# Performance work log

Hardware: AMD Instinct MI355X
Metric: run time of the kernel (lower is better)

The kernel has to match this reference:

```python
import jax, jax.numpy as jnp
import numpy as np

D_MODEL = 1024
N_HEADS = 16
D_HEAD = D_MODEL // N_HEADS
WINDOW = 128
D_FF = 3 * D_MODEL
EPS = 1e-5


def _layer_norm(x, g, b):
    mu = jnp.mean(x, axis=-1, keepdims=True)
    var = jnp.var(x, axis=-1, keepdims=True)
    return (x - mu) * jax.lax.rsqrt(var + EPS) * g + b


def setup_inputs() -> dict:
    key = jax.random.key(0)
    ks = jax.random.split(key, 10)
    B, S = 2, 2048
    sd = 0.02
    return {
        "x": jax.random.normal(ks[0], (B, S, D_MODEL), dtype=jnp.float32),
        "w_qkv": jax.random.normal(ks[1], (D_MODEL, 3 * D_MODEL), dtype=jnp.float32) * sd,
        "b_qkv": jnp.zeros((3 * D_MODEL,), jnp.float32),
        "w_out": jax.random.normal(ks[2], (D_MODEL, D_MODEL), dtype=jnp.float32) * sd,
        "b_out": jnp.zeros((D_MODEL,), jnp.float32),
        "w_ff1": jax.random.normal(ks[3], (D_MODEL, D_FF), dtype=jnp.float32) * sd,
        "b_ff1": jnp.zeros((D_FF,), jnp.float32),
        "w_ff2": jax.random.normal(ks[4], (D_FF, D_MODEL), dtype=jnp.float32) * sd,
        "b_ff2": jnp.zeros((D_MODEL,), jnp.float32),
        "ln1_g": jnp.ones((D_MODEL,), jnp.float32),
        "ln1_b": jnp.zeros((D_MODEL,), jnp.float32),
        "ln2_g": jnp.ones((D_MODEL,), jnp.float32),
        "ln2_b": jnp.zeros((D_MODEL,), jnp.float32),
    }


def reference(x, w_qkv, b_qkv, w_out, b_out, w_ff1, b_ff1, w_ff2, b_ff2,
              ln1_g, ln1_b, ln2_g, ln2_b):
    B, S, D = x.shape
    h = _layer_norm(x, ln1_g, ln1_b)
    qkv = (h @ w_qkv + b_qkv).reshape(B, S, 3, N_HEADS, D_HEAD)
    q, k, v = (jnp.moveaxis(qkv[:, :, i], 1, 2) for i in range(3))  # (B,H,S,dh)
    scores = jnp.einsum('bhqd,bhkd->bhqk', q, k) / jnp.sqrt(jnp.float32(D_HEAD))
    i = jnp.arange(S)[:, None]
    j = jnp.arange(S)[None, :]
    allowed = (j <= i) & (j > i - WINDOW)  # causal sliding window band
    scores = jnp.where(allowed, scores, -jnp.inf)
    attn = jax.nn.softmax(scores, axis=-1)
    ctx = jnp.einsum('bhqk,bhkd->bqhd', attn, v).reshape(B, S, D)
    x = x + (ctx @ w_out + b_out)
    h2 = _layer_norm(x, ln2_g, ln2_b)
    ff = jax.nn.gelu(h2 @ w_ff1 + b_ff1, approximate=False) @ w_ff2 + b_ff2
    return x + ff
```

## Files before the change

### kernel.cpp

```cpp
#include <hip/hip_runtime.h>

#define D_MODEL 1024
#define SEQ 2048
#define BATCH 2
#define NH 16
#define DH 64
#define WIN 128
#define DFF 3072

typedef __bf16 bf16x8 __attribute__((ext_vector_type(8)));
typedef float f32x4 __attribute__((ext_vector_type(4)));
typedef unsigned short u16;
typedef unsigned int u32;

__device__ __forceinline__ float b2f(u16 u) {
    unsigned int x = ((unsigned int)u) << 16;
    return __uint_as_float(x);
}
__device__ __forceinline__ u16 f2b(float f) {
    unsigned int x = __float_as_uint(f);
    x += 0x7fffu + ((x >> 16) & 1u);
    return (u16)(x >> 16);
}
__device__ __forceinline__ u32 pk2(float a, float b) {
    return (u32)f2b(a) | ((u32)f2b(b) << 16);
}

__global__ __launch_bounds__(256) void transpose_cvt_k(
        const float* __restrict__ in, u16* __restrict__ out, int R, int C) {
    __shared__ u16 tile[32][33];
    int tx = threadIdx.x & 31;
    int ty = threadIdx.x >> 5;
    int r0 = blockIdx.y * 32, c0 = blockIdx.x * 32;
#pragma unroll
    for (int i = 0; i < 4; ++i)
        tile[ty + i * 8][tx] = f2b(in[(size_t)(r0 + ty + i * 8) * C + c0 + tx]);
    __syncthreads();
#pragma unroll
    for (int i = 0; i < 4; ++i)
        out[(size_t)(c0 + ty + i * 8) * R + r0 + tx] = tile[tx][ty + i * 8];
}

__global__ __launch_bounds__(256) void ln_k(
        const float* __restrict__ x, const float* __restrict__ g,
        const float* __restrict__ bta, u16* __restrict__ out) {
    int row = blockIdx.x;
    const float* xr = x + (size_t)row * D_MODEL;
    float v[4];
    float sum = 0.f, sq = 0.f;
#pragma unroll
    for (int i = 0; i < 4; ++i) {
        v[i] = xr[threadIdx.x + i * 256];
        sum += v[i];
        sq += v[i] * v[i];
    }
#pragma unroll
    for (int off = 32; off > 0; off >>= 1) {
        sum += __shfl_xor(sum, off, 64);
        sq  += __shfl_xor(sq, off, 64);
    }
    __shared__ float s1[4], s2[4];
    int w = threadIdx.x >> 6;
    if ((threadIdx.x & 63) == 0) { s1[w] = sum; s2[w] = sq; }
    __syncthreads();
    sum = s1[0] + s1[1] + s1[2] + s1[3];
    sq  = s2[0] + s2[1] + s2[2] + s2[3];
    float mu = sum * (1.f / D_MODEL);
    float var = sq * (1.f / D_MODEL) - mu * mu;
    float rstd = rsqrtf(var + 1e-5f);
    u16* outr = out + (size_t)row * D_MODEL;
#pragma unroll
    for (int i = 0; i < 4; ++i) {
        int c = threadIdx.x + i * 256;
        outr[c] = f2b((v[i] - mu) * rstd * g[c] + bta[c]);
    }
}

template <int GELU, int RESID, int OUTF32, int VSPLIT>
__global__ __launch_bounds__(256) void gemm_k(
        const u16* __restrict__ A, const u16* __restrict__ Bt,
        const float* __restrict__ bias, const float* __restrict__ resid,
        void* __restrict__ Cv, u16* __restrict__ vt,
        int M, int N, int K, int ldc) {
    __shared__ u16 As[128 * 64];
    __shared__ u16 Bs[128 * 64];
    int tid = threadIdx.x;
    int w = tid >> 6, lane = tid & 63;
    int qd = lane >> 4, l15 = lane & 15;

    int lin = blockIdx.x;
    int xcd = lin & 7, idx = lin >> 3;
    int m0 = (xcd * 4 + (idx & 3)) * 128;
    int n0 = (idx >> 2) * 128;

    const u16* gsrc[8];
    u16* ldst[8];
#pragma unroll
    for (int i = 0; i < 8; ++i) {
        int c = w * 8 + i;
        int cb = c & 15;
        int row = cb * 8 + (lane >> 3);
        int cg = (lane & 7) ^ (row & 7);
        gsrc[i] = (c < 16 ? A + (size_t)(m0 + row) * K
                          : Bt + (size_t)(n0 + row) * K) + cg * 8;
        ldst[i] = (c < 16 ? As : Bs) + cb * 512;
    }

    int wm = w & 1, wn = w >> 1;
    f32x4 acc[4][4];
#pragma unroll
    for (int mt = 0; mt < 4; ++mt)
#pragma unroll
        for (int nt = 0; nt < 4; ++nt)
            acc[mt][nt] = (f32x4){0.f, 0.f, 0.f, 0.f};

    int aoff[4][2], boff[4][2];
#pragma unroll
    for (int t = 0; t < 4; ++t) {
        int ar = wm * 64 + t * 16 + l15;
        int br = wn * 64 + t * 16 + l15;
#pragma unroll
        for (int h = 0; h < 2; ++h) {
            aoff[t][h] = ar * 64 + (((h * 4 + qd) ^ (ar & 7)) * 8);
            boff[t][h] = br * 64 + (((h * 4 + qd) ^ (br & 7)) * 8);
        }
    }

    for (int k0 = 0; k0 < K; k0 += 64) {
        __syncthreads();
#pragma unroll
        for (int i = 0; i < 8; ++i)
            __builtin_amdgcn_global_load_lds(
                (__attribute__((address_space(1))) void*)(gsrc[i] + k0),
                (__attribute__((address_space(3))) void*)(ldst[i]), 16, 0, 0);
        __syncthreads();
        bf16x8 av[4][2], bv[4][2];
#pragma unroll
        for (int t = 0; t < 4; ++t)
#pragma unroll
            for (int h = 0; h < 2; ++h) {
                av[t][h] = *(const bf16x8*)&As[aoff[t][h]];
                bv[t][h] = *(const bf16x8*)&Bs[boff[t][h]];
            }
#pragma unroll
        for (int mt = 0; mt < 4; ++mt)
#pragma unroll
            for (int nt = 0; nt < 4; ++nt) {
                acc[mt][nt] = __builtin_amdgcn_mfma_f32_16x16x32_bf16(
                    av[mt][0], bv[nt][0], acc[mt][nt], 0, 0, 0);
                acc[mt][nt] = __builtin_amdgcn_mfma_f32_16x16x32_bf16(
                    av[mt][1], bv[nt][1], acc[mt][nt], 0, 0, 0);
            }
    }

#pragma unroll
    for (int mt = 0; mt < 4; ++mt) {
        int row0 = m0 + wm * 64 + mt * 16 + qd * 4;
#pragma unroll
        for (int nt = 0; nt < 4; ++nt) {
            int col = n0 + wn * 64 + nt * 16 + l15;
            float v[4];
#pragma unroll
            for (int reg = 0; reg < 4; ++reg) {
                v[reg] = acc[mt][nt][reg] + bias[col];
                if (GELU) v[reg] = 0.5f * v[reg] * (1.f + erff(v[reg] * 0.70710678118654752f));
                if (RESID) v[reg] += resid[(size_t)(row0 + reg) * ldc + col];
            }
            if (VSPLIT && col >= 2 * D_MODEL) {
                int d = col - 2 * D_MODEL;
                int bh = (row0 >> 11) * NH + (d >> 6);
                ushort4 pkv = {f2b(v[0]), f2b(v[1]), f2b(v[2]), f2b(v[3])};
                *(ushort4*)&vt[((size_t)(bh * DH + (d & 63))) * SEQ + (row0 & (SEQ - 1))] = pkv;
            } else {
#pragma unroll
                for (int reg = 0; reg < 4; ++reg) {
                    if (OUTF32) ((float*)Cv)[(size_t)(row0 + reg) * ldc + col] = v[reg];
                    else        ((u16*)Cv)[(size_t)(row0 + reg) * ldc + col] = f2b(v[reg]);
                }
            }
        }
    }
}

__global__ __launch_bounds__(256) void attn_k(
        const u16* __restrict__ qk, const u16* __restrict__ vt,
        u16* __restrict__ ctx) {
    int lane = threadIdx.x & 63, l15 = lane & 15, quad = lane >> 4;
    int t = blockIdx.x * 4 + (threadIdx.x >> 6);
    int qt = t & (SEQ / 16 - 1);
    int h  = (t >> 7) & (NH - 1);
    int b  = t >> 11;
    int q0 = qt * 16;
    int bh = b * NH + h;

    const u16* qrow = qk + (size_t)(b * SEQ + q0 + l15) * (2 * D_MODEL) + h * DH + quad * 8;
    bf16x8 qf0 = *(const bf16x8*)(qrow);
    bf16x8 qf1 = *(const bf16x8*)(qrow + 32);
    const u16* kbase = qk + (size_t)(b * SEQ) * (2 * D_MODEL) + D_MODEL + h * DH + quad * 8;
    const u16* vbase = vt + (size_t)(bh * DH) * SEQ;

    f32x4 o[4] = {{0.f, 0.f, 0.f, 0.f}, {0.f, 0.f, 0.f, 0.f},
                  {0.f, 0.f, 0.f, 0.f}, {0.f, 0.f, 0.f, 0.f}};
    float m = -1e30f, l = 0.f;
    int q = q0 + l15;
    int cs = q0 - (WIN - 1);
    cs = cs < 0 ? 0 : (cs & ~31);

    for (int c = cs; c <= q0 + 15; c += 32) {
        const u16* k0p = kbase + (size_t)(c + l15) * (2 * D_MODEL);
        const u16* k1p = k0p + (size_t)16 * (2 * D_MODEL);
        bf16x8 ka0 = *(const bf16x8*)(k0p);
        bf16x8 ka1 = *(const bf16x8*)(k0p + 32);
        bf16x8 kb0 = *(const bf16x8*)(k1p);
        bf16x8 kb1 = *(const bf16x8*)(k1p + 32);
        f32x4 s0 = {0.f, 0.f, 0.f, 0.f}, s1 = {0.f, 0.f, 0.f, 0.f};
        s0 = __builtin_amdgcn_mfma_f32_16x16x32_bf16(ka0, qf0, s0, 0, 0, 0);
        s0 = __builtin_amdgcn_mfma_f32_16x16x32_bf16(ka1, qf1, s0, 0, 0, 0);
        s1 = __builtin_amdgcn_mfma_f32_16x16x32_bf16(kb0, qf0, s1, 0, 0, 0);
        s1 = __builtin_amdgcn_mfma_f32_16x16x32_bf16(kb1, qf1, s1, 0, 0, 0);

        float p0[4], p1[4];
        float cm = -1e30f;
#pragma unroll
        for (int reg = 0; reg < 4; ++reg) {
            int k0i = c + quad * 4 + reg;
            p0[reg] = ((unsigned)(q - k0i) < WIN) ? s0[reg] * 0.125f : -1e30f;
            p1[reg] = ((unsigned)(q - k0i - 16) < WIN) ? s1[reg] * 0.125f : -1e30f;
            cm = fmaxf(cm, fmaxf(p0[reg], p1[reg]));
        }
        cm = fmaxf(cm, __shfl_xor(cm, 16, 64));
        cm = fmaxf(cm, __shfl_xor(cm, 32, 64));
        float mn = fmaxf(m, cm);
        float alpha = __expf(m - mn);
        m = mn;
        float ls = 0.f;
#pragma unroll
        for (int reg = 0; reg < 4; ++reg) {
            p0[reg] = __expf(p0[reg] - mn);
            p1[reg] = __expf(p1[reg] - mn);
            ls += p0[reg] + p1[reg];
        }
        ls += __shfl_xor(ls, 16, 64);
        ls += __shfl_xor(ls, 32, 64);
        l = l * alpha + ls;
#pragma unroll
        for (int mt = 0; mt < 4; ++mt) o[mt] *= alpha;

        u32 z0 = pk2(p0[0], p0[1]), z1 = pk2(p0[2], p0[3]);
        u32 w0 = pk2(p1[0], p1[1]), w1 = pk2(p1[2], p1[3]);
        int slo = ((quad & 1) * 2) * 16 + l15;
        int shi = slo + 16;
        u32 zl0 = (u32)__shfl((int)z0, slo, 64), zl1 = (u32)__shfl((int)z1, slo, 64);
        u32 zh0 = (u32)__shfl((int)z0, shi, 64), zh1 = (u32)__shfl((int)z1, shi, 64);
        u32 wl0 = (u32)__shfl((int)w0, slo, 64), wl1 = (u32)__shfl((int)w1, slo, 64);
        u32 wh0 = (u32)__shfl((int)w0, shi, 64), wh1 = (u32)__shfl((int)w1, shi, 64);
        alignas(16) u32 pr[4];
        pr[0] = quad < 2 ? zl0 : wl0;
        pr[1] = quad < 2 ? zl1 : wl1;
        pr[2] = quad < 2 ? zh0 : wh0;
        pr[3] = quad < 2 ? zh1 : wh1;
        bf16x8 pf = *(const bf16x8*)pr;

#pragma unroll
        for (int mt = 0; mt < 4; ++mt) {
            bf16x8 vf = *(const bf16x8*)(vbase + (size_t)(mt * 16 + l15) * SEQ + c + quad * 8);
            o[mt] = __builtin_amdgcn_mfma_f32_16x16x32_bf16(vf, pf, o[mt], 0, 0, 0);
        }
    }

    float rdiv = 1.f / l;
    u16* crow = ctx + (size_t)(b * SEQ + q0 + l15) * D_MODEL + h * DH;
#pragma unroll
    for (int mt = 0; mt < 4; ++mt) {
        ushort4 pkv = {f2b(o[mt][0] * rdiv), f2b(o[mt][1] * rdiv),
                       f2b(o[mt][2] * rdiv), f2b(o[mt][3] * rdiv)};
        *(ushort4*)(crow + mt * 16 + quad * 4) = pkv;
    }
}

extern "C" void kernel_launch(void* const* d_in, const int* in_sizes, int n_in,
                              void* d_out, int out_size, void* d_ws, size_t ws_size,
                              hipStream_t stream) {
    (void)in_sizes; (void)n_in; (void)out_size; (void)ws_size;
    const float* x     = (const float*)d_in[0];
    const float* w_qkv = (const float*)d_in[1];
    const float* b_qkv = (const float*)d_in[2];
    const float* w_out = (const float*)d_in[3];
    const float* b_out = (const float*)d_in[4];
    const float* w_ff1 = (const float*)d_in[5];
    const float* b_ff1 = (const float*)d_in[6];
    const float* w_ff2 = (const float*)d_in[7];
    const float* b_ff2 = (const float*)d_in[8];
    const float* ln1g  = (const float*)d_in[9];
    const float* ln1b  = (const float*)d_in[10];
    const float* ln2g  = (const float*)d_in[11];
    const float* ln2b  = (const float*)d_in[12];
    float* out = (float*)d_out;

    const int M = BATCH * SEQ;
    char* base = (char*)d_ws;
    u16*   hbf   = (u16*)(base);
    u16*   qkbuf = (u16*)(base + (8ll  << 20));
    u16*   ctxbf = (u16*)(base + (24ll << 20));
    u16*   vtbuf = (u16*)(base + (32ll << 20));
    u16*   ffbf  = (u16*)(base + (8ll  << 20));
    float* x2    = (float*)(base + (40ll << 20));
    u16*   wqkvT = (u16*)(base + (56ll << 20));
    u16*   woutT = (u16*)(base + (62ll << 20));
    u16*   wff1T = (u16*)(base + (64ll << 20));
    u16*   wff2T = (u16*)(base + (70ll << 20));

    transpose_cvt_k<<<dim3(3 * D_MODEL / 32, D_MODEL / 32), 256, 0, stream>>>(w_qkv, wqkvT, D_MODEL, 3 * D_MODEL);
    transpose_cvt_k<<<dim3(D_MODEL / 32, D_MODEL / 32), 256, 0, stream>>>(w_out, woutT, D_MODEL, D_MODEL);
    transpose_cvt_k<<<dim3(DFF / 32, D_MODEL / 32), 256, 0, stream>>>(w_ff1, wff1T, D_MODEL, DFF);
    transpose_cvt_k<<<dim3(D_MODEL / 32, DFF / 32), 256, 0, stream>>>(w_ff2, wff2T, DFF, D_MODEL);

    ln_k<<<M, 256, 0, stream>>>(x, ln1g, ln1b, hbf);
    gemm_k<0, 0, 0, 1><<<dim3((3 * D_MODEL / 128) * 32), 256, 0, stream>>>(
        hbf, wqkvT, b_qkv, nullptr, qkbuf, vtbuf, M, 3 * D_MODEL, D_MODEL, 2 * D_MODEL);
    attn_k<<<dim3(BATCH * NH * (SEQ / 16) / 4), 256, 0, stream>>>(qkbuf, vtbuf, ctxbf);
    gemm_k<0, 1, 1, 0><<<dim3((D_MODEL / 128) * 32), 256, 0, stream>>>(
        ctxbf, woutT, b_out, x, x2, nullptr, M, D_MODEL, D_MODEL, D_MODEL);
    ln_k<<<M, 256, 0, stream>>>(x2, ln2g, ln2b, hbf);
    gemm_k<1, 0, 0, 0><<<dim3((DFF / 128) * 32), 256, 0, stream>>>(
        hbf, wff1T, b_ff1, nullptr, ffbf, nullptr, M, DFF, D_MODEL, DFF);
    gemm_k<0, 1, 1, 0><<<dim3((D_MODEL / 128) * 32), 256, 0, stream>>>(
        ffbf, wff2T, b_ff2, x2, out, nullptr, M, D_MODEL, DFF, D_MODEL);
}
```

Measured before the change: 314.9 us.

## Pipeline GEMM global-to-LDS loads with a 4-stage K=32 ring buffer

The GEMM main loop now keeps a four-slot LDS ring of 32-wide K slices and prefetches three steps ahead using direct global-to-LDS loads. Partial vmcnt waits and a single barrier per step replace the previous load-then-sync pattern. This is meant to hide global memory latency behind MFMA work. In exchange, each step does half the MFMA work per barrier, and the LDS footprint doubles to 64KB, which may lower occupancy.

```diff
diff --git a/kernel.cpp b/kernel.cpp
--- a/kernel.cpp
+++ b/kernel.cpp
@@ -25,6 +25,10 @@
 __device__ __forceinline__ u32 pk2(float a, float b) {
     return (u32)f2b(a) | ((u32)f2b(b) << 16);
 }
+
+#define WAIT_VMCNT0() __builtin_amdgcn_s_waitcnt(0x0F70)
+#define WAIT_VMCNT4() __builtin_amdgcn_s_waitcnt(0x0F74)
+#define WAIT_VMCNT8() __builtin_amdgcn_s_waitcnt(0x0F78)
 
 __global__ __launch_bounds__(256) void transpose_cvt_k(
         const float* __restrict__ in, u16* __restrict__ out, int R, int C) {
@@ -82,8 +86,8 @@
         const float* __restrict__ bias, const float* __restrict__ resid,
         void* __restrict__ Cv, u16* __restrict__ vt,
         int M, int N, int K, int ldc) {
-    __shared__ u16 As[128 * 64];
-    __shared__ u16 Bs[128 * 64];
+    __shared__ u16 As[4 * 4096];
+    __shared__ u16 Bs[4 * 4096];
     int tid = threadIdx.x;
     int w = tid >> 6, lane = tid & 63;
     int qd = lane >> 4, l15 = lane & 15;
@@ -93,17 +97,17 @@
     int m0 = (xcd * 4 + (idx & 3)) * 128;
     int n0 = (idx >> 2) * 128;
 
-    const u16* gsrc[8];
-    u16* ldst[8];
-#pragma unroll
-    for (int i = 0; i < 8; ++i) {
-        int c = w * 8 + i;
-        int cb = c & 15;
-        int row = cb * 8 + (lane >> 3);
-        int cg = (lane & 7) ^ (row & 7);
-        gsrc[i] = (c < 16 ? A + (size_t)(m0 + row) * K
-                          : Bt + (size_t)(n0 + row) * K) + cg * 8;
-        ldst[i] = (c < 16 ? As : Bs) + cb * 512;
+    const u16* gsrc[4];
+    u16* ldst[4];
+#pragma unroll
+    for (int i = 0; i < 4; ++i) {
+        int c = w * 4 + i;
+        int cb = c & 7;
+        int row = cb * 16 + (lane >> 2);
+        int cg = (lane & 3) ^ ((row >> 1) & 3);
+        gsrc[i] = (c < 8 ? A + (size_t)(m0 + row) * K
+                         : Bt + (size_t)(n0 + row) * K) + cg * 8;
+        ldst[i] = (c < 8 ? As : Bs) + cb * 512;
     }
 
     int wm = w & 1, wn = w >> 1;
@@ -114,43 +118,54 @@
         for (int nt = 0; nt < 4; ++nt)
             acc[mt][nt] = (f32x4){0.f, 0.f, 0.f, 0.f};
 
-    int aoff[4][2], boff[4][2];
+    int aoff[4], boff[4];
 #pragma unroll
     for (int t = 0; t < 4; ++t) {
         int ar = wm * 64 + t * 16 + l15;
         int br = wn * 64 + t * 16 + l15;
-#pragma unroll
-        for (int h = 0; h < 2; ++h) {
-            aoff[t][h] = ar * 64 + (((h * 4 + qd) ^ (ar & 7)) * 8);
-            boff[t][h] = br * 64 + (((h * 4 + qd) ^ (br & 7)) * 8);
-        }
-    }
-
-    for (int k0 = 0; k0 < K; k0 += 64) {
-        __syncthreads();
-#pragma unroll
-        for (int i = 0; i < 8; ++i)
+        aoff[t] = ar * 32 + ((qd ^ ((ar >> 1) & 3)) * 8);
+        boff[t] = br * 32 + ((qd ^ ((br >> 1) & 3)) * 8);
+    }
+
+    int nsteps = K >> 5;
+#pragma unroll
+    for (int t = 0; t < 3; ++t)
+#pragma unroll
+        for (int i = 0; i < 4; ++i)
             __builtin_amdgcn_global_load_lds(
-                (__attribute__((address_space(1))) void*)(gsrc[i] + k0),
-                (__attribute__((address_space(3))) void*)(ldst[i]), 16, 0, 0);
-        __syncthreads();
-        bf16x8 av[4][2], bv[4][2];
-#pragma unroll
-        for (int t = 0; t < 4; ++t)
-#pragma unroll
-            for (int h = 0; h < 2; ++h) {
-                av[t][h] = *(const bf16x8*)&As[aoff[t][h]];
-                bv[t][h] = *(const bf16x8*)&Bs[boff[t][h]];
-            }
+                (__attribute__((address_space(1))) void*)(gsrc[i] + (t << 5)),
+                (__attribute__((address_space(3))) void*)(ldst[i] + t * 4096),
+                16, 0, 0);
+
+    for (int s = 0; s < nsteps; ++s) {
+        int rem = nsteps - 1 - s;
+        if (rem >= 2)      WAIT_VMCNT8();
+        else if (rem == 1) WAIT_VMCNT4();
+        else               WAIT_VMCNT0();
+        __builtin_amdgcn_s_barrier();
+        if (s + 3 < nsteps) {
+            int k0 = (s + 3) << 5;
+            int pre = ((s + 3) & 3) * 4096;
+#pragma unroll
+            for (int i = 0; i < 4; ++i)
+                __builtin_amdgcn_global_load_lds(
+                    (__attribute__((address_space(1))) void*)(gsrc[i] + k0),
+                    (__attribute__((address_space(3))) void*)(ldst[i] + pre),
+                    16, 0, 0);
+        }
+        int cur = (s & 3) * 4096;
+        bf16x8 av[4], bv[4];
+#pragma unroll
+        for (int t = 0; t < 4; ++t) {
+            av[t] = *(const bf16x8*)&As[aoff[t] + cur];
+            bv[t] = *(const bf16x8*)&Bs[boff[t] + cur];
+        }
 #pragma unroll
         for (int mt = 0; mt < 4; ++mt)
 #pragma unroll
-            for (int nt = 0; nt < 4; ++nt) {
+            for (int nt = 0; nt < 4; ++nt)
                 acc[mt][nt] = __builtin_amdgcn_mfma_f32_16x16x32_bf16(
-                    av[mt][0], bv[nt][0], acc[mt][nt], 0, 0, 0);
-                acc[mt][nt] = __builtin_amdgcn_mfma_f32_16x16x32_bf16(
-                    av[mt][1], bv[nt][1], acc[mt][nt], 0, 0, 0);
-            }
+                    av[mt], bv[nt], acc[mt][nt], 0, 0, 0);
     }
 
 #pragma unroll
```

New measurement: 292.7 us. -7.0%, faster.
